# Performance work log

Measured on AMD Instinct MI355X. Metric: run time of the kernel, lower is better.

## Reference

```python
import jax, jax.numpy as jnp
import numpy as np

B, L, D, V, K = 4, 2048, 1024, 32, 4096  # batch, seq, embedding_dim, vq_dim, num_embeddings


def setup_inputs() -> dict:
    key = jax.random.key(0)
    k0, k1, k2, k3 = jax.random.split(key, 4)
    h = jax.random.normal(k0, (B, L, D), jnp.float32)
    attn_mask = jnp.ones((B, L), jnp.float32)
    # proj: Linear(D -> V); proj_inv: Linear(V -> D)
    Wp = jax.random.normal(k1, (V, D), jnp.float32) / np.float32(np.sqrt(D))
    bp = jnp.zeros((V,), jnp.float32)
    Wpi = jax.random.normal(k2, (D, V), jnp.float32) / np.float32(np.sqrt(V))
    bpi = jnp.zeros((D,), jnp.float32)
    # embedding init uniform(-1/K, 1/K)
    emb = jax.random.uniform(k3, (K, V), jnp.float32, -1.0 / K, 1.0 / K)
    return {"h": h, "attn_mask": attn_mask, "Wp": Wp, "bp": bp,
            "Wpi": Wpi, "bpi": bpi, "emb": emb}


def reference(h, attn_mask, Wp, bp, Wpi, bpi, emb, temperature=1.0):
    # project + L2 normalize
    hp = jnp.einsum('bld,vd->blv', h, Wp) + bp            # [B,L,V]
    hp = hp / jnp.linalg.norm(hp, axis=-1, keepdims=True)
    # normalize codebook (in torch this is an in-place .data update)
    emb_n = emb / jnp.linalg.norm(emb, axis=-1, keepdims=True)  # [K,V]
    # squared euclidean distances hp vs codebook
    d = (jnp.sum(hp * hp, axis=-1, keepdims=True)
         + jnp.sum(emb_n * emb_n, axis=-1)
         - 2.0 * jnp.einsum('blv,kv->blk', hp, emb_n))    # [B,L,K]
    A = jax.nn.softmax(-d / temperature, axis=-1)         # [B,L,K]
    code = jnp.argmax(A, axis=-1)                         # [B,L]
    h_vq = jnp.einsum('blk,kv->blv', A, emb_n)            # train mode: A @ embedding
    # masked scatter into zeros is equivalent to masking out unselected positions
    m = (attn_mask == 1)
    quantized = jnp.where(m[..., None], h_vq, jnp.float32(0.0))
    vq_code = jnp.where(m, code, 0).astype(jnp.int32)
    quantized = jnp.einsum('blv,dv->bld', quantized, Wpi) + bpi
    vq_loss = jnp.float32(0.0)
    return quantized, vq_code, vq_loss
```

## Files before the change

kernel.cpp:

```cpp
#include <hip/hip_runtime.h>
#include <hip/hip_bf16.h>
#include <math.h>

#define NTOK 8192
#define DIM  1024
#define VDIM 32
#define KCODES 4096

#define SC 2.8853900817779268f

typedef __attribute__((ext_vector_type(8))) short short8;
typedef __attribute__((ext_vector_type(4))) float f32x4;
typedef __attribute__((ext_vector_type(2))) float f32x2;

#define MFMA16(A,B,C) __builtin_amdgcn_mfma_f32_16x16x32_bf16(A, B, C, 0, 0, 0)

__device__ __forceinline__ unsigned short f2bf(float x) {
    unsigned u = __builtin_bit_cast(unsigned, x);
    u += 0x7FFF + ((u >> 16) & 1);
    return (unsigned short)(u >> 16);
}
__device__ __forceinline__ float bf2f(unsigned short b) {
    unsigned u = ((unsigned)b) << 16;
    return __builtin_bit_cast(float, u);
}
__device__ __forceinline__ float fexp2(float x) {
#if __has_builtin(__builtin_amdgcn_exp2f)
    return __builtin_amdgcn_exp2f(x);
#else
    return __expf(0.6931471805599453f * x);
#endif
}

struct U4 { unsigned x, y, z, w; };

__device__ __forceinline__ void split8(const float* p, short8* H, short8* L) {
    unsigned hh[4], ll[4];
    #pragma unroll
    for (int i = 0; i < 4; ++i) {
        unsigned short a = f2bf(p[2 * i]);
        unsigned short b = f2bf(p[2 * i + 1]);
        hh[i] = (unsigned)a | ((unsigned)b << 16);
        unsigned short la = f2bf(p[2 * i] - bf2f(a));
        unsigned short lb = f2bf(p[2 * i + 1] - bf2f(b));
        ll[i] = (unsigned)la | ((unsigned)lb << 16);
    }
    U4 uh = {hh[0], hh[1], hh[2], hh[3]};
    U4 ul = {ll[0], ll[1], ll[2], ll[3]};
    *H = __builtin_bit_cast(short8, uh);
    *L = __builtin_bit_cast(short8, ul);
}

__device__ __forceinline__ short8 pack8(const float* p) {
    unsigned u[8];
    #pragma unroll
    for (int j = 0; j < 8; ++j) u[j] = __builtin_bit_cast(unsigned, p[j]) + 0x8000u;
    U4 uh;
    uh.x = __builtin_amdgcn_perm(u[1], u[0], 0x07060302);
    uh.y = __builtin_amdgcn_perm(u[3], u[2], 0x07060302);
    uh.z = __builtin_amdgcn_perm(u[5], u[4], 0x07060302);
    uh.w = __builtin_amdgcn_perm(u[7], u[6], 0x07060302);
    return __builtin_bit_cast(short8, uh);
}

__device__ __forceinline__ int lsw(int row, int j) {
    int s = ((row >> 1) ^ (row >> 3)) & 3;
    return row * 40 + ((j ^ s) * 8);
}

#define OFS_E_HI   0
#define OFS_E_LO   131072
#define OFS_ET_HI  262144
#define OFS_WPI_HI 458752
#define OFS_WPI_LO 491520
#define OFS_HP_HI  524288
#define OFS_HP_LO  786432
#define F32_BASE   1048576
#define NSPLIT 8
#define FOFS_HVP 0
#define FOFS_LP  2097152
#define FOFS_AMP 2162688
#define FOFS_AIP 2228224

__global__ __launch_bounds__(256) void k_proj(const float* __restrict__ h,
                                              const float* __restrict__ Wp,
                                              const float* __restrict__ bp,
                                              const float* __restrict__ emb,
                                              const float* __restrict__ Wpi,
                                              unsigned short* __restrict__ W,
                                              unsigned short* __restrict__ hp_hi,
                                              unsigned short* __restrict__ hp_lo,
                                              float* __restrict__ loss_out) {
    __shared__ __align__(16) float red[4][16][36];
    __shared__ __align__(16) unsigned short Th[32][72];
    int tid = threadIdx.x;
    if (blockIdx.x >= 512) {
        int bid2 = blockIdx.x - 512;
        if (bid2 < 64) {
            int cb = bid2 * 64;
            int c = tid >> 2, s = tid & 3;
            const float* src = emb + (size_t)(cb + c) * VDIM + s * 8;
            float4 a = *(const float4*)src;
            float4 b = *(const float4*)(src + 4);
            float ps = a.x*a.x + a.y*a.y + a.z*a.z + a.w*a.w
                     + b.x*b.x + b.y*b.y + b.z*b.z + b.w*b.w;
            ps += __shfl_xor(ps, 1);
            ps += __shfl_xor(ps, 2);
            float inv = 1.0f / sqrtf(ps);
            float vals[8] = {a.x*inv, a.y*inv, a.z*inv, a.w*inv,
                             b.x*inv, b.y*inv, b.z*inv, b.w*inv};
            short8 H, L;
            split8(vals, &H, &L);
            *(short8*)(W + OFS_E_HI + (size_t)(cb + c) * VDIM + s * 8) = H;
            *(short8*)(W + OFS_E_LO + (size_t)(cb + c) * VDIM + s * 8) = L;
            #pragma unroll
            for (int j = 0; j < 8; ++j) Th[s * 8 + j][c] = f2bf(vals[j]);
            __syncthreads();
            int row = tid >> 3, seg = tid & 7;
            *(short8*)(W + OFS_ET_HI + (size_t)row * KCODES + cb + seg * 8) =
                *(const short8*)&Th[row][seg * 8];
            if (bid2 == 0 && tid == 0) loss_out[0] = 0.0f;
        } else {
            int i0 = (bid2 - 64) * 2048 + tid * 8;
            float4 a = *(const float4*)(Wpi + i0);
            float4 b = *(const float4*)(Wpi + i0 + 4);
            float vals[8] = {a.x, a.y, a.z, a.w, b.x, b.y, b.z, b.w};
            short8 H, L;
            split8(vals, &H, &L);
            *(short8*)(W + OFS_WPI_HI + i0) = H;
            *(short8*)(W + OFS_WPI_LO + i0) = L;
        }
        return;
    }
    int w = tid >> 6, l = tid & 63, q = l >> 4, m = l & 15;
    int tok0 = blockIdx.x * 16;
    const f32x4 zero4 = {0.f, 0.f, 0.f, 0.f};
    f32x4 acc0 = zero4, acc1 = zero4;
    const float* hb = h + (size_t)(tok0 + m) * DIM + w * 256 + q * 8;
    const float* wp0 = Wp + (size_t)m * DIM + w * 256 + q * 8;
    const float* wp1 = wp0 + (size_t)16 * DIM;
    #pragma unroll
    for (int c = 0; c < 8; ++c) {
        float4 a = *(const float4*)(hb + c * 32);
        float4 b = *(const float4*)(hb + c * 32 + 4);
        float va[8] = {a.x, a.y, a.z, a.w, b.x, b.y, b.z, b.w};
        short8 Bh, Bl;
        split8(va, &Bh, &Bl);
        float4 w0a = *(const float4*)(wp0 + c * 32);
        float4 w0b = *(const float4*)(wp0 + c * 32 + 4);
        float v0[8] = {w0a.x, w0a.y, w0a.z, w0a.w, w0b.x, w0b.y, w0b.z, w0b.w};
        short8 A0h, A0l;
        split8(v0, &A0h, &A0l);
        float4 w1a = *(const float4*)(wp1 + c * 32);
        float4 w1b = *(const float4*)(wp1 + c * 32 + 4);
        float v1[8] = {w1a.x, w1a.y, w1a.z, w1a.w, w1b.x, w1b.y, w1b.z, w1b.w};
        short8 A1h, A1l;
        split8(v1, &A1h, &A1l);
        acc0 = MFMA16(A0l, Bl, acc0); acc0 = MFMA16(A0l, Bh, acc0);
        acc0 = MFMA16(A0h, Bl, acc0); acc0 = MFMA16(A0h, Bh, acc0);
        acc1 = MFMA16(A1l, Bl, acc1); acc1 = MFMA16(A1l, Bh, acc1);
        acc1 = MFMA16(A1h, Bl, acc1); acc1 = MFMA16(A1h, Bh, acc1);
    }
    *(f32x4*)&red[w][m][4 * q]      = acc0;
    *(f32x4*)&red[w][m][16 + 4 * q] = acc1;
    __syncthreads();
    #pragma unroll
    for (int half = 0; half < 2; ++half) {
        int t = (tid >> 5) + half * 8, v = tid & 31;
        float s = bp[v];
        #pragma unroll
        for (int j = 0; j < 4; ++j) s += red[j][t][v];
        float sq = s * s;
        #pragma unroll
        for (int off = 1; off < 32; off <<= 1) sq += __shfl_xor(sq, off);
        float nv = s * (SC / sqrtf(sq));
        unsigned short hb2 = f2bf(nv);
        size_t idx = (size_t)(tok0 + t) * VDIM + v;
        hp_hi[idx] = hb2;
        hp_lo[idx] = f2bf(nv - bf2f(hb2));
    }
}

__global__ __launch_bounds__(256, 2) void k_vq(const unsigned short* __restrict__ W,
                                               float* __restrict__ hvp,
                                               float* __restrict__ lp,
                                               float* __restrict__ amp,
                                               int* __restrict__ aip) {
    __shared__ __align__(16) unsigned short Eh[2][64 * 40];
    __shared__ __align__(16) unsigned short El[2][64 * 40];

    const unsigned short* E_hi  = W + OFS_E_HI;
    const unsigned short* E_lo  = W + OFS_E_LO;
    const unsigned short* Et_hi = W + OFS_ET_HI;
    const unsigned short* hp_hi = W + OFS_HP_HI;
    const unsigned short* hp_lo = W + OFS_HP_LO;

    int tid = threadIdx.x;
    int w = tid >> 6, l = tid & 63, q = l >> 4, m = l & 15;
    int tg = blockIdx.x >> 3, sp = blockIdx.x & 7;
    int tok0 = tg * 128 + w * 32;
    int cb0 = sp * 512;
    int sig = ((m & 12) << 1) | (m & 3);
    const f32x4 zero4 = {0.f, 0.f, 0.f, 0.f};

    int cs = tid >> 2, js = tid & 3;
    int lds_off = lsw(cs, js);
    size_t gs = (size_t)cs * VDIM + js * 8;

    size_t h0 = (size_t)(tok0 + m) * VDIM + q * 8;
    short8 hph0 = *(const short8*)(hp_hi + h0);
    short8 hpl0 = *(const short8*)(hp_lo + h0);
    short8 hph1 = *(const short8*)(hp_hi + h0 + 16 * VDIM);
    short8 hpl1 = *(const short8*)(hp_lo + h0 + 16 * VDIM);

    {
        size_t tb = (size_t)cb0 * VDIM;
        short8 a = *(const short8*)(E_hi + tb + gs);
        short8 b = *(const short8*)(E_lo + tb + gs);
        *(short8*)&Eh[0][lds_off] = a;
        *(short8*)&El[0][lds_off] = b;
    }
    __syncthreads();

    f32x4 hv00 = zero4, hv01 = zero4, hv10 = zero4, hv11 = zero4;
    f32x2 ls0v = {0.f, 0.f}, ls1v = {0.f, 0.f};
    float am0 = -1e30f, am1 = -1e30f;
    int ai0 = 0, ai1 = 0;

    #pragma unroll 1
    for (int t = 0; t < 8; ++t) {
        int buf = t & 1;
        short8 sa, sb;
        if (t < 7) {
            size_t tb = (size_t)(cb0 + (t + 1) * 64) * VDIM;
            sa = *(const short8*)(E_hi + tb + gs);
            sb = *(const short8*)(E_lo + tb + gs);
        }
        int cbase = cb0 + t * 64;
        size_t tb0 = (size_t)sig * KCODES + cbase + q * 8;
        short8 T00 = *(const short8*)(Et_hi + tb0);
        short8 T01 = *(const short8*)(Et_hi + tb0 + (size_t)4 * KCODES);
        short8 T10 = *(const short8*)(Et_hi + tb0 + 32);
        short8 T11 = *(const short8*)(Et_hi + tb0 + 32 + (size_t)4 * KCODES);
        short8 E00h = *(const short8*)&Eh[buf][lsw(sig,          q)];
        short8 E00l = *(const short8*)&El[buf][lsw(sig,          q)];
        short8 E01h = *(const short8*)&Eh[buf][lsw(sig + 4,      q)];
        short8 E01l = *(const short8*)&El[buf][lsw(sig + 4,      q)];
        short8 E10h = *(const short8*)&Eh[buf][lsw(32 + sig,     q)];
        short8 E10l = *(const short8*)&El[buf][lsw(32 + sig,     q)];
        short8 E11h = *(const short8*)&Eh[buf][lsw(32 + sig + 4, q)];
        short8 E11l = *(const short8*)&El[buf][lsw(32 + sig + 4, q)];

        f32x4 sA0, sA1, sB0, sB1, sC0, sC1, sD0, sD1;
        sA0 = MFMA16(E00h, hpl0, zero4);
        sA1 = MFMA16(E01h, hpl0, zero4);
        sB0 = MFMA16(E00h, hpl1, zero4);
        sB1 = MFMA16(E01h, hpl1, zero4);
        sC0 = MFMA16(E10h, hpl0, zero4);
        sC1 = MFMA16(E11h, hpl0, zero4);
        sD0 = MFMA16(E10h, hpl1, zero4);
        sD1 = MFMA16(E11h, hpl1, zero4);
        sA0 = MFMA16(E00l, hph0, sA0);
        sA1 = MFMA16(E01l, hph0, sA1);
        sB0 = MFMA16(E00l, hph1, sB0);
        sB1 = MFMA16(E01l, hph1, sB1);
        sC0 = MFMA16(E10l, hph0, sC0);
        sC1 = MFMA16(E11l, hph0, sC1);
        sD0 = MFMA16(E10l, hph1, sD0);
        sD1 = MFMA16(E11l, hph1, sD1);
        sA0 = MFMA16(E00h, hph0, sA0);
        sA1 = MFMA16(E01h, hph0, sA1);
        sB0 = MFMA16(E00h, hph1, sB0);
        sB1 = MFMA16(E01h, hph1, sB1);
        sC0 = MFMA16(E10h, hph0, sC0);
        sC1 = MFMA16(E11h, hph0, sC1);
        sD0 = MFMA16(E10h, hph1, sD0);
        sD1 = MFMA16(E11h, hph1, sD1);

        {
            int lbase = cbase + 8 * q;
            float p[8];
            #pragma unroll
            for (int r = 0; r < 4; ++r) { p[r] = fexp2(sA0[r]); p[4 + r] = fexp2(sA1[r]); }
            short8 Ph = pack8(p);
            hv00 = MFMA16(T00, Ph, hv00);
            hv01 = MFMA16(T01, Ph, hv01);
            #pragma unroll
            for (int r = 0; r < 4; ++r) {
                float sv = sA0[r];
                if (sv > am0) { am0 = sv; ai0 = lbase + r; }
                sv = sA1[r];
                if (sv > am0) { am0 = sv; ai0 = lbase + 4 + r; }
            }
            f32x2 pa = {p[0], p[1]}, pb = {p[2], p[3]};
            f32x2 pc = {p[4], p[5]}, pd = {p[6], p[7]};
            ls0v += (pa + pb) + (pc + pd);
        }
        {
            int lbase = cbase + 8 * q;
            float p[8];
            #pragma unroll
            for (int r = 0; r < 4; ++r) { p[r] = fexp2(sB0[r]); p[4 + r] = fexp2(sB1[r]); }
            short8 Ph = pack8(p);
            hv10 = MFMA16(T00, Ph, hv10);
            hv11 = MFMA16(T01, Ph, hv11);
            #pragma unroll
            for (int r = 0; r < 4; ++r) {
                float sv = sB0[r];
                if (sv > am1) { am1 = sv; ai1 = lbase + r; }
                sv = sB1[r];
                if (sv > am1) { am1 = sv; ai1 = lbase + 4 + r; }
            }
            f32x2 pa = {p[0], p[1]}, pb = {p[2], p[3]};
            f32x2 pc = {p[4], p[5]}, pd = {p[6], p[7]};
            ls1v += (pa + pb) + (pc + pd);
        }
        {
            int lbase = cbase + 32 + 8 * q;
            float p[8];
            #pragma unroll
            for (int r = 0; r < 4; ++r) { p[r] = fexp2(sC0[r]); p[4 + r] = fexp2(sC1[r]); }
            short8 Ph = pack8(p);
            hv00 = MFMA16(T10, Ph, hv00);
            hv01 = MFMA16(T11, Ph, hv01);
            #pragma unroll
            for (int r = 0; r < 4; ++r) {
                float sv = sC0[r];
                if (sv > am0) { am0 = sv; ai0 = lbase + r; }
                sv = sC1[r];
                if (sv > am0) { am0 = sv; ai0 = lbase + 4 + r; }
            }
            f32x2 pa = {p[0], p[1]}, pb = {p[2], p[3]};
            f32x2 pc = {p[4], p[5]}, pd = {p[6], p[7]};
            ls0v += (pa + pb) + (pc + pd);
        }
        {
            int lbase = cbase + 32 + 8 * q;
            float p[8];
            #pragma unroll
            for (int r = 0; r < 4; ++r) { p[r] = fexp2(sD0[r]); p[4 + r] = fexp2(sD1[r]); }
            short8 Ph = pack8(p);
            hv10 = MFMA16(T10, Ph, hv10);
            hv11 = MFMA16(T11, Ph, hv11);
            #pragma unroll
            for (int r = 0; r < 4; ++r) {
                float sv = sD0[r];
                if (sv > am1) { am1 = sv; ai1 = lbase + r; }
                sv = sD1[r];
                if (sv > am1) { am1 = sv; ai1 = lbase + 4 + r; }
            }
            f32x2 pa = {p[0], p[1]}, pb = {p[2], p[3]};
            f32x2 pc = {p[4], p[5]}, pd = {p[6], p[7]};
            ls1v += (pa + pb) + (pc + pd);
        }

        if (t < 7) {
            int nb = buf ^ 1;
            *(short8*)&Eh[nb][lds_off] = sa;
            *(short8*)&El[nb][lds_off] = sb;
            __syncthreads();
        }
    }

    float ls0 = ls0v.x + ls0v.y;
    float ls1 = ls1v.x + ls1v.y;
    #pragma unroll
    for (int off = 16; off <= 32; off <<= 1) {
        ls0 += __shfl_xor(ls0, off);
        float a2 = __shfl_xor(am0, off);
        int   i2 = __shfl_xor(ai0, off);
        if (a2 > am0 || (a2 == am0 && i2 < ai0)) { am0 = a2; ai0 = i2; }
        ls1 += __shfl_xor(ls1, off);
        a2 = __shfl_xor(am1, off);
        i2 = __shfl_xor(ai1, off);
        if (a2 > am1 || (a2 == am1 && i2 < ai1)) { am1 = a2; ai1 = i2; }
    }
    size_t gtok = (size_t)sp * NTOK + tok0;
    if (q == 0) {
        lp[gtok + m] = ls0;      amp[gtok + m] = am0;      aip[gtok + m] = ai0;
        lp[gtok + 16 + m] = ls1; amp[gtok + 16 + m] = am1; aip[gtok + 16 + m] = ai1;
    }
    float* dst0 = hvp + (gtok + m) * VDIM;
    *(f32x4*)(dst0 + 8 * q)     = hv00;
    *(f32x4*)(dst0 + 8 * q + 4) = hv01;
    float* dst1 = hvp + (gtok + 16 + m) * VDIM;
    *(f32x4*)(dst1 + 8 * q)     = hv10;
    *(f32x4*)(dst1 + 8 * q + 4) = hv11;
}

__global__ __launch_bounds__(256) void k_out(const unsigned short* __restrict__ W,
                                             const float* __restrict__ mask,
                                             const float* __restrict__ bpi,
                                             const float* __restrict__ hvp,
                                             const float* __restrict__ lp,
                                             const float* __restrict__ amp,
                                             const int* __restrict__ aip,
                                             float* __restrict__ out,
                                             float* __restrict__ code_out) {
    __shared__ float invl[32];
    __shared__ float lred[32][9];
    __shared__ float amred[32][9];
    __shared__ int   aired[32][9];
    __shared__ __align__(16) unsigned short hvh[32][40];
    __shared__ __align__(16) unsigned short hvl[32][40];
    const unsigned short* Wpi_hi = W + OFS_WPI_HI;
    const unsigned short* Wpi_lo = W + OFS_WPI_LO;
    int tid = threadIdx.x;
    int tok0 = blockIdx.x * 32;
    const f32x4 zero4 = {0.f, 0.f, 0.f, 0.f};

    {
        int t = tid >> 3, s = tid & 7;
        size_t gi = (size_t)s * NTOK + tok0 + t;
        lred[t][s]  = lp[gi];
        amred[t][s] = amp[gi];
        aired[t][s] = aip[gi];
    }
    __syncthreads();
    if (tid < 32) {
        float L = 0.f, A = -1e30f;
        int I = 0x7fffffff;
        #pragma unroll
        for (int s = 0; s < NSPLIT; ++s) {
            L += lred[tid][s];
            float a2 = amred[tid][s];
            int   i2 = aired[tid][s];
            if (a2 > A || (a2 == A && i2 < I)) { A = a2; I = i2; }
        }
        bool on = (mask[tok0 + tid] == 1.0f);
        code_out[tok0 + tid] = on ? (float)I : 0.0f;
        invl[tid] = on ? (1.0f / L) : 0.0f;
    }
    __syncthreads();
    {
        int t = tid >> 3, g = tid & 7;
        f32x4 x = zero4;
        #pragma unroll
        for (int sp = 0; sp < NSPLIT; ++sp)
            x += *(const f32x4*)&hvp[((size_t)sp * NTOK + tok0 + t) * VDIM + g * 4];
        float iv = invl[t];
        #pragma unroll
        for (int j = 0; j < 4; ++j) {
            float xv = x[j] * iv;
            unsigned short hb = f2bf(xv);
            hvh[t][g * 4 + j] = hb;
            hvl[t][g * 4 + j] = f2bf(xv - bf2f(hb));
        }
    }
    __syncthreads();
    int w = tid >> 6, l = tid & 63, q = l >> 4, m = l & 15;
    short8 gh0 = *(const short8*)&hvh[m][q * 8];
    short8 gl0 = *(const short8*)&hvl[m][q * 8];
    short8 gh1 = *(const short8*)&hvh[16 + m][q * 8];
    short8 gl1 = *(const short8*)&hvl[16 + m][q * 8];
    #pragma unroll
    for (int dt = 0; dt < 16; ++dt) {
        int dbase = w * 256 + dt * 16;
        short8 Ah = *(const short8*)(Wpi_hi + (size_t)(dbase + m) * VDIM + q * 8);
        short8 Al = *(const short8*)(Wpi_lo + (size_t)(dbase + m) * VDIM + q * 8);
        float4 bias = *(const float4*)(bpi + dbase + 4 * q);
        f32x4 o0 = MFMA16(Al, gh0, zero4);
        o0 = MFMA16(Ah, gl0, o0);
        o0 = MFMA16(Ah, gh0, o0);
        f32x4 o1 = MFMA16(Al, gh1, zero4);
        o1 = MFMA16(Ah, gl1, o1);
        o1 = MFMA16(Ah, gh1, o1);
        float4 r0 = make_float4(o0[0] + bias.x, o0[1] + bias.y,
                                o0[2] + bias.z, o0[3] + bias.w);
        *(float4*)(out + (size_t)(tok0 + m) * DIM + dbase + 4 * q) = r0;
        float4 r1 = make_float4(o1[0] + bias.x, o1[1] + bias.y,
                                o1[2] + bias.z, o1[3] + bias.w);
        *(float4*)(out + (size_t)(tok0 + 16 + m) * DIM + dbase + 4 * q) = r1;
    }
}

extern "C" void kernel_launch(void* const* d_in, const int* in_sizes, int n_in,
                              void* d_out, int out_size, void* d_ws, size_t ws_size,
                              hipStream_t stream) {
    const float* h    = (const float*)d_in[0];
    const float* mask = (const float*)d_in[1];
    const float* Wp   = (const float*)d_in[2];
    const float* bp   = (const float*)d_in[3];
    const float* Wpi  = (const float*)d_in[4];
    const float* bpi  = (const float*)d_in[5];
    const float* emb  = (const float*)d_in[6];
    float* out = (float*)d_out;

    unsigned short* W = (unsigned short*)d_ws;
    unsigned short* hp_hi = W + OFS_HP_HI;
    unsigned short* hp_lo = W + OFS_HP_LO;
    float* fbase = (float*)(W + F32_BASE);
    float* hvp = fbase + FOFS_HVP;
    float* lpp = fbase + FOFS_LP;
    float* ampp = fbase + FOFS_AMP;
    int*   aipp = (int*)(fbase + FOFS_AIP);

    float* code_out = out + (size_t)NTOK * DIM;
    float* loss_out = code_out + NTOK;

    hipLaunchKernelGGL(k_proj, dim3(592), dim3(256), 0, stream, h, Wp, bp, emb, Wpi, W, hp_hi, hp_lo, loss_out);
    hipLaunchKernelGGL(k_vq,   dim3(512), dim3(256), 0, stream, W, hvp, lpp, ampp, aipp);
    hipLaunchKernelGGL(k_out,  dim3(256), dim3(256), 0, stream, W, mask, bpi, hvp, lpp, ampp, aipp, out, code_out);
}
```

Baseline: 128.3 us.

## Fuse output projection into VQ kernel via last-block atomic counter

```diff
diff --git a/kernel.cpp b/kernel.cpp
--- a/kernel.cpp
+++ b/kernel.cpp
@@ -81,6 +81,7 @@
 #define FOFS_LP  2097152
 #define FOFS_AMP 2162688
 #define FOFS_AIP 2228224
+#define FOFS_CNT 2293760
 
 __global__ __launch_bounds__(256) void k_proj(const float* __restrict__ h,
                                               const float* __restrict__ Wp,
@@ -90,6 +91,7 @@
                                               unsigned short* __restrict__ W,
                                               unsigned short* __restrict__ hp_hi,
                                               unsigned short* __restrict__ hp_lo,
+                                              int* __restrict__ cnt,
                                               float* __restrict__ loss_out) {
     __shared__ __align__(16) float red[4][16][36];
     __shared__ __align__(16) unsigned short Th[32][72];
@@ -97,6 +99,10 @@
     if (blockIdx.x >= 512) {
         int bid2 = blockIdx.x - 512;
         if (bid2 < 64) {
+            if (bid2 == 0) {
+                cnt[tid] = 0;
+                if (tid == 0) loss_out[0] = 0.0f;
+            }
             int cb = bid2 * 64;
             int c = tid >> 2, s = tid & 3;
             const float* src = emb + (size_t)(cb + c) * VDIM + s * 8;
@@ -119,7 +125,6 @@
             int row = tid >> 3, seg = tid & 7;
             *(short8*)(W + OFS_ET_HI + (size_t)row * KCODES + cb + seg * 8) =
                 *(const short8*)&Th[row][seg * 8];
-            if (bid2 == 0 && tid == 0) loss_out[0] = 0.0f;
         } else {
             int i0 = (bid2 - 64) * 2048 + tid * 8;
             float4 a = *(const float4*)(Wpi + i0);
@@ -185,9 +190,21 @@
                                                float* __restrict__ hvp,
                                                float* __restrict__ lp,
                                                float* __restrict__ amp,
-                                               int* __restrict__ aip) {
+                                               int* __restrict__ aip,
+                                               const float* __restrict__ mask,
+                                               const float* __restrict__ bpi,
+                                               int* __restrict__ cnt,
+                                               float* __restrict__ out,
+                                               float* __restrict__ code_out) {
     __shared__ __align__(16) unsigned short Eh[2][64 * 40];
     __shared__ __align__(16) unsigned short El[2][64 * 40];
+    __shared__ float invl[32];
+    __shared__ float lred[32][9];
+    __shared__ float amred[32][9];
+    __shared__ int   aired[32][9];
+    __shared__ __align__(16) unsigned short hvh[32][40];
+    __shared__ __align__(16) unsigned short hvl[32][40];
+    __shared__ int lastflag[4];
 
     const unsigned short* E_hi  = W + OFS_E_HI;
     const unsigned short* E_lo  = W + OFS_E_LO;
@@ -386,91 +403,84 @@
     float* dst1 = hvp + (gtok + 16 + m) * VDIM;
     *(f32x4*)(dst1 + 8 * q)     = hv10;
     *(f32x4*)(dst1 + 8 * q + 4) = hv11;
-}
-
-__global__ __launch_bounds__(256) void k_out(const unsigned short* __restrict__ W,
-                                             const float* __restrict__ mask,
-                                             const float* __restrict__ bpi,
-                                             const float* __restrict__ hvp,
-                                             const float* __restrict__ lp,
-                                             const float* __restrict__ amp,
-                                             const int* __restrict__ aip,
-                                             float* __restrict__ out,
-                                             float* __restrict__ code_out) {
-    __shared__ float invl[32];
-    __shared__ float lred[32][9];
-    __shared__ float amred[32][9];
-    __shared__ int   aired[32][9];
-    __shared__ __align__(16) unsigned short hvh[32][40];
-    __shared__ __align__(16) unsigned short hvl[32][40];
+
+    __threadfence();
+    __syncthreads();
+    if (tid < 4)
+        lastflag[tid] = (atomicAdd(&cnt[tg * 4 + tid], 1) == NSPLIT - 1);
+    __syncthreads();
+    if (!(lastflag[0] | lastflag[1] | lastflag[2] | lastflag[3])) return;
+    __threadfence();
+
     const unsigned short* Wpi_hi = W + OFS_WPI_HI;
     const unsigned short* Wpi_lo = W + OFS_WPI_LO;
-    int tid = threadIdx.x;
-    int tok0 = blockIdx.x * 32;
-    const f32x4 zero4 = {0.f, 0.f, 0.f, 0.f};
-
-    {
-        int t = tid >> 3, s = tid & 7;
-        size_t gi = (size_t)s * NTOK + tok0 + t;
-        lred[t][s]  = lp[gi];
-        amred[t][s] = amp[gi];
-        aired[t][s] = aip[gi];
-    }
-    __syncthreads();
-    if (tid < 32) {
-        float L = 0.f, A = -1e30f;
-        int I = 0x7fffffff;
+    #pragma unroll 1
+    for (int g = 0; g < 4; ++g) {
+        if (!lastflag[g]) continue;
+        int tok0o = tg * 128 + g * 32;
+        {
+            int t2 = tid >> 3, s2 = tid & 7;
+            size_t gi = (size_t)s2 * NTOK + tok0o + t2;
+            lred[t2][s2]  = lp[gi];
+            amred[t2][s2] = amp[gi];
+            aired[t2][s2] = aip[gi];
+        }
+        __syncthreads();
+        if (tid < 32) {
+            float L = 0.f, A = -1e30f;
+            int I = 0x7fffffff;
+            #pragma unroll
+            for (int s2 = 0; s2 < NSPLIT; ++s2) {
+                L += lred[tid][s2];
+                float a2 = amred[tid][s2];
+                int   i2 = aired[tid][s2];
+                if (a2 > A || (a2 == A && i2 < I)) { A = a2; I = i2; }
+            }
+            bool on = (mask[tok0o + tid] == 1.0f);
+            code_out[tok0o + tid] = on ? (float)I : 0.0f;
+            invl[tid] = on ? (1.0f / L) : 0.0f;
+        }
+        __syncthreads();
+        {
+            int t2 = tid >> 3, g2 = tid & 7;
+            f32x4 x = zero4;
+            #pragma unroll
+            for (int s2 = 0; s2 < NSPLIT; ++s2)
+                x += *(const f32x4*)&hvp[((size_t)s2 * NTOK + tok0o + t2) * VDIM + g2 * 4];
+            float iv = invl[t2];
+            #pragma unroll
+            for (int j = 0; j < 4; ++j) {
+                float xv = x[j] * iv;
+                unsigned short hb = f2bf(xv);
+                hvh[t2][g2 * 4 + j] = hb;
+                hvl[t2][g2 * 4 + j] = f2bf(xv - bf2f(hb));
+            }
+        }
+        __syncthreads();
+        short8 gh0 = *(const short8*)&hvh[m][q * 8];
+        short8 gl0 = *(const short8*)&hvl[m][q * 8];
+        short8 gh1 = *(const short8*)&hvh[16 + m][q * 8];
+        short8 gl1 = *(const short8*)&hvl[16 + m][q * 8];
         #pragma unroll
-        for (int s = 0; s < NSPLIT; ++s) {
-            L += lred[tid][s];
-            float a2 = amred[tid][s];
-            int   i2 = aired[tid][s];
-            if (a2 > A || (a2 == A && i2 < I)) { A = a2; I = i2; }
-        }
-        bool on = (mask[tok0 + tid] == 1.0f);
-        code_out[tok0 + tid] = on ? (float)I : 0.0f;
-        invl[tid] = on ? (1.0f / L) : 0.0f;
-    }
-    __syncthreads();
-    {
-        int t = tid >> 3, g = tid & 7;
-        f32x4 x = zero4;
-        #pragma unroll
-        for (int sp = 0; sp < NSPLIT; ++sp)
-            x += *(const f32x4*)&hvp[((size_t)sp * NTOK + tok0 + t) * VDIM + g * 4];
-        float iv = invl[t];
-        #pragma unroll
-        for (int j = 0; j < 4; ++j) {
-            float xv = x[j] * iv;
-            unsigned short hb = f2bf(xv);
-            hvh[t][g * 4 + j] = hb;
-            hvl[t][g * 4 + j] = f2bf(xv - bf2f(hb));
-        }
-    }
-    __syncthreads();
-    int w = tid >> 6, l = tid & 63, q = l >> 4, m = l & 15;
-    short8 gh0 = *(const short8*)&hvh[m][q * 8];
-    short8 gl0 = *(const short8*)&hvl[m][q * 8];
-    short8 gh1 = *(const short8*)&hvh[16 + m][q * 8];
-    short8 gl1 = *(const short8*)&hvl[16 + m][q * 8];
-    #pragma unroll
-    for (int dt = 0; dt < 16; ++dt) {
-        int dbase = w * 256 + dt * 16;
-        short8 Ah = *(const short8*)(Wpi_hi + (size_t)(dbase + m) * VDIM + q * 8);
-        short8 Al = *(const short8*)(Wpi_lo + (size_t)(dbase + m) * VDIM + q * 8);
-        float4 bias = *(const float4*)(bpi + dbase + 4 * q);
-        f32x4 o0 = MFMA16(Al, gh0, zero4);
-        o0 = MFMA16(Ah, gl0, o0);
-        o0 = MFMA16(Ah, gh0, o0);
-        f32x4 o1 = MFMA16(Al, gh1, zero4);
-        o1 = MFMA16(Ah, gl1, o1);
-        o1 = MFMA16(Ah, gh1, o1);
-        float4 r0 = make_float4(o0[0] + bias.x, o0[1] + bias.y,
-                                o0[2] + bias.z, o0[3] + bias.w);
-        *(float4*)(out + (size_t)(tok0 + m) * DIM + dbase + 4 * q) = r0;
-        float4 r1 = make_float4(o1[0] + bias.x, o1[1] + bias.y,
-                                o1[2] + bias.z, o1[3] + bias.w);
-        *(float4*)(out + (size_t)(tok0 + 16 + m) * DIM + dbase + 4 * q) = r1;
+        for (int dt = 0; dt < 16; ++dt) {
+            int dbase = w * 256 + dt * 16;
+            short8 Ah = *(const short8*)(Wpi_hi + (size_t)(dbase + m) * VDIM + q * 8);
+            short8 Al = *(const short8*)(Wpi_lo + (size_t)(dbase + m) * VDIM + q * 8);
+            float4 bias = *(const float4*)(bpi + dbase + 4 * q);
+            f32x4 o0 = MFMA16(Al, gh0, zero4);
+            o0 = MFMA16(Ah, gl0, o0);
+            o0 = MFMA16(Ah, gh0, o0);
+            f32x4 o1 = MFMA16(Al, gh1, zero4);
+            o1 = MFMA16(Ah, gl1, o1);
+            o1 = MFMA16(Ah, gh1, o1);
+            float4 r0 = make_float4(o0[0] + bias.x, o0[1] + bias.y,
+                                    o0[2] + bias.z, o0[3] + bias.w);
+            *(float4*)(out + (size_t)(tok0o + m) * DIM + dbase + 4 * q) = r0;
+            float4 r1 = make_float4(o1[0] + bias.x, o1[1] + bias.y,
+                                    o1[2] + bias.z, o1[3] + bias.w);
+            *(float4*)(out + (size_t)(tok0o + 16 + m) * DIM + dbase + 4 * q) = r1;
+        }
+        __syncthreads();
     }
 }
 
@@ -494,11 +504,11 @@
     float* lpp = fbase + FOFS_LP;
     float* ampp = fbase + FOFS_AMP;
     int*   aipp = (int*)(fbase + FOFS_AIP);
+    int*   cntp = (int*)(fbase + FOFS_CNT);
 
     float* code_out = out + (size_t)NTOK * DIM;
     float* loss_out = code_out + NTOK;
 
-    hipLaunchKernelGGL(k_proj, dim3(592), dim3(256), 0, stream, h, Wp, bp, emb, Wpi, W, hp_hi, hp_lo, loss_out);
-    hipLaunchKernelGGL(k_vq,   dim3(512), dim3(256), 0, stream, W, hvp, lpp, ampp, aipp);
-    hipLaunchKernelGGL(k_out,  dim3(256), dim3(256), 0, stream, W, mask, bpi, hvp, lpp, ampp, aipp, out, code_out);
-}
+    hipLaunchKernelGGL(k_proj, dim3(592), dim3(256), 0, stream, h, Wp, bp, emb, Wpi, W, hp_hi, hp_lo, cntp, loss_out);
+    hipLaunchKernelGGL(k_vq,   dim3(512), dim3(256), 0, stream, W, hvp, lpp, ampp, aipp, mask, bpi, cntp, out, code_out);
+}
```

New measurement: 250.2 us. +95.0%, slower.
